# Performance work log

Measured on AMD Instinct MI355X. Metric: run time of the kernel, lower is better.

Reference implementation:

```python
import jax, jax.numpy as jnp
import numpy as np

B, S, C_IN, C_OUT = 8, 2048, 512, 512

def setup_inputs() -> dict:
    key = jax.random.key(0)
    k1, k2, k3, k4 = jax.random.split(key, 4)
    sc = 1.0 / np.sqrt(C_IN)
    return {
        "x": jax.random.normal(k1, (B, S, C_IN), dtype=jnp.float32),
        "Wq": jax.random.normal(k2, (C_OUT, C_IN), dtype=jnp.float32) * sc,
        "Wk": jax.random.normal(k3, (C_OUT, C_IN), dtype=jnp.float32) * sc,
        "Wv": jax.random.normal(k4, (C_OUT, C_IN), dtype=jnp.float32) * sc,
    }

def reference(x, Wq, Wk, Wv):
    # x: [B,S,Cin]; weights [Cout,Cin] (torch Linear convention, no bias)
    C = Wq.shape[0]
    dk = jnp.sqrt(jnp.float32(1.0) / C)  # torch: sqrt(1/out_features)
    q = jnp.einsum('bsi,oi->bso', x, Wq)
    k = jnp.einsum('bsi,oi->bso', x, Wk)
    v = jnp.einsum('bsi,oi->bso', x, Wv)
    phi_q = jax.nn.elu(q * dk) + 1.0
    phi_k = jax.nn.elu(k * dk) + 1.0
    b = x.shape[0]
    mem0 = jnp.zeros((b, C, C), x.dtype)   # running sum of phi_k v^T
    zeta0 = jnp.zeros((b, C), x.dtype)     # running sum of phi_k
    def step(carry, inp):
        mem, zeta = carry
        pq, pk, vv = inp                    # each [B,C]
        dm = pk[:, :, None] * vv[:, None, :]              # [B,C,C]
        scale = jnp.einsum('bc,bc->b', pq, pk + zeta) + 1e-5
        num = jnp.einsum('bc,bcd->bd', pq, dm + mem)
        y = num / scale[:, None]
        # state updates are under torch.no_grad -> detach
        new_mem = jax.lax.stop_gradient(mem + dm)
        new_zeta = jax.lax.stop_gradient(zeta + pk)
        return (new_mem, new_zeta), y
    xs = (phi_q.transpose(1, 0, 2), phi_k.transpose(1, 0, 2), v.transpose(1, 0, 2))
    _, ys = jax.lax.scan(step, (mem0, zeta0), xs)  # ys: [S,B,C]
    return ys.transpose(1, 0, 2)                   # [B,S,C]
```

## Files before the change

### kernel.cpp

```cpp
#include <hip/hip_runtime.h>


constexpr int Bn  = 8;
constexpr int Sn  = 2048;
constexpr int Cn  = 512;
constexpr int Tn  = 128;
constexpr int NCn = 16;
constexpr float DKf = 0.04419417382415922f;

typedef __attribute__((ext_vector_type(8))) short bf16x8;
typedef __attribute__((ext_vector_type(4))) float f32x4;

__device__ __forceinline__ unsigned short f2bf(float f) {
  unsigned u = __float_as_uint(f);
  u = (u + 0x7fffu + ((u >> 16) & 1u)) >> 16;
  return (unsigned short)u;
}
__device__ __forceinline__ float bf2f(unsigned short h) {
  return __uint_as_float(((unsigned)h) << 16);
}
__device__ __forceinline__ float phi_f(float u) {
  float s = u * DKf;
  return s > 0.0f ? s + 1.0f : __expf(s);
}

__device__ __forceinline__ void stage128x32(const unsigned short* __restrict__ g,
                                            int ld, unsigned short* lds,
                                            int wid, int lane) {
#pragma unroll
  for (int cc = 0; cc < 2; ++cc) {
    const int row = cc * 64 + wid * 16 + (lane >> 2);
    const int ks  = (lane & 3) ^ ((row >> 1) & 3);
    const unsigned short* src = g + (size_t)row * ld + ks * 8;
    unsigned short* dst = lds + (size_t)(cc * 256 + wid * 64) * 8;
    __builtin_amdgcn_global_load_lds(
        (const __attribute__((address_space(1))) void*)src,
        (__attribute__((address_space(3))) void*)dst, 16, 0, 0);
  }
}

__device__ __forceinline__ void mm_loop(const unsigned short* __restrict__ Ag, int lda,
                                        const unsigned short* __restrict__ Bg, int ldb,
                                        int nkt,
                                        unsigned short* Al, unsigned short* Bl,
                                        f32x4 acc[4][4]) {
  const int t = threadIdx.x, wid = t >> 6, lane = t & 63;
  const int wm = wid >> 1, wn = wid & 1;
  const int fr = lane & 15, kb = lane >> 4;
  for (int kt = 0; kt < nkt; ++kt) {
    __syncthreads();
    stage128x32(Ag + kt * 32, lda, Al, wid, lane);
    stage128x32(Bg + kt * 32, ldb, Bl, wid, lane);
    __syncthreads();
    bf16x8 af[4], bf[4];
#pragma unroll
    for (int m = 0; m < 4; ++m) {
      const int r = wm * 64 + m * 16 + fr;
      af[m] = *(const bf16x8*)&Al[r * 32 + ((kb ^ ((r >> 1) & 3)) << 3)];
    }
#pragma unroll
    for (int n = 0; n < 4; ++n) {
      const int r = wn * 64 + n * 16 + fr;
      bf[n] = *(const bf16x8*)&Bl[r * 32 + ((kb ^ ((r >> 1) & 3)) << 3)];
    }
#pragma unroll
    for (int m = 0; m < 4; ++m)
#pragma unroll
      for (int n = 0; n < 4; ++n)
        acc[m][n] = __builtin_amdgcn_mfma_f32_16x16x32_bf16(af[m], bf[n], acc[m][n], 0, 0, 0);
  }
}

__global__ __launch_bounds__(256) void k_cast_x(const float* __restrict__ x,
                                                unsigned short* __restrict__ xb) {
  const size_t i8 = ((size_t)blockIdx.x * 256 + threadIdx.x) * 8;
  float4 a = *(const float4*)&x[i8];
  float4 b = *(const float4*)&x[i8 + 4];
  uint4 o;
  o.x = (unsigned)f2bf(a.x) | ((unsigned)f2bf(a.y) << 16);
  o.y = (unsigned)f2bf(a.z) | ((unsigned)f2bf(a.w) << 16);
  o.z = (unsigned)f2bf(b.x) | ((unsigned)f2bf(b.y) << 16);
  o.w = (unsigned)f2bf(b.z) | ((unsigned)f2bf(b.w) << 16);
  *(uint4*)&xb[i8] = o;
}

__global__ __launch_bounds__(256) void k_cast_w(const float* __restrict__ Wq,
                                                const float* __restrict__ Wk,
                                                const float* __restrict__ Wv,
                                                unsigned short* __restrict__ Wb) {
  const int z = blockIdx.y;
  const float* __restrict__ src = (z == 0) ? Wq : (z == 1 ? Wk : Wv);
  const size_t i8 = ((size_t)blockIdx.x * 256 + threadIdx.x) * 8;
  float4 a = *(const float4*)&src[i8];
  float4 b = *(const float4*)&src[i8 + 4];
  uint4 o;
  o.x = (unsigned)f2bf(a.x) | ((unsigned)f2bf(a.y) << 16);
  o.y = (unsigned)f2bf(a.z) | ((unsigned)f2bf(a.w) << 16);
  o.z = (unsigned)f2bf(b.x) | ((unsigned)f2bf(b.y) << 16);
  o.w = (unsigned)f2bf(b.z) | ((unsigned)f2bf(b.w) << 16);
  *(uint4*)&Wb[(size_t)z * Cn * Cn + i8] = o;
}

__global__ __launch_bounds__(256) void k_proj(
    const unsigned short* __restrict__ xb, const unsigned short* __restrict__ Wb,
    unsigned short* __restrict__ PQ, unsigned short* __restrict__ PK,
    unsigned short* __restrict__ PKt, unsigned short* __restrict__ Vt,
    float* __restrict__ zsum)
{
  __shared__ unsigned short Al[128 * 32], Bl[128 * 32];
  __shared__ float zbuf[2][128];
  const int bid = blockIdx.x;
  const int xcd = bid & 7, idx = bid >> 3;
  const int n = idx & 3, z = (idx >> 2) % 3, mloc = idx / 12;
  const int n0 = n * 128, m0 = (xcd * 16 + mloc) * 128;
  const int t = threadIdx.x, wid = t >> 6, lane = t & 63;
  const int wm = wid >> 1, wn = wid & 1;
  f32x4 acc[4][4];
  const f32x4 zero = {0.f, 0.f, 0.f, 0.f};
#pragma unroll
  for (int m = 0; m < 4; ++m)
#pragma unroll
    for (int nn = 0; nn < 4; ++nn) acc[m][nn] = zero;

  mm_loop(xb + (size_t)m0 * Cn, Cn,
          Wb + (size_t)z * Cn * Cn + (size_t)n0 * Cn, Cn, Cn / 32, Al, Bl, acc);

  float ps[4] = {0.f, 0.f, 0.f, 0.f};
#pragma unroll
  for (int m = 0; m < 4; ++m)
#pragma unroll
    for (int nn = 0; nn < 4; ++nn) {
      const int row0 = m0 + wm * 64 + m * 16 + ((lane >> 4) << 2);
      const int col  = n0 + wn * 64 + nn * 16 + (lane & 15);
      f32x4 v = acc[m][nn];
      if (z == 0) {
#pragma unroll
        for (int j = 0; j < 4; ++j)
          PQ[(size_t)(row0 + j) * Cn + col] = f2bf(phi_f(v[j]));
      } else if (z == 1) {
        ushort4 p;
#pragma unroll
        for (int j = 0; j < 4; ++j) {
          unsigned short u = f2bf(phi_f(v[j]));
          PK[(size_t)(row0 + j) * Cn + col] = u;
          (&p.x)[j] = u;
          ps[nn] += bf2f(u);
        }
        const int b = row0 >> 11, tq = row0 & (Sn - 1);
        *(ushort4*)&PKt[((size_t)b * Cn + col) * Sn + tq] = p;
      } else {
        ushort4 p;
#pragma unroll
        for (int j = 0; j < 4; ++j) (&p.x)[j] = f2bf(v[j]);
        const int b = row0 >> 11, tq = row0 & (Sn - 1);
        *(ushort4*)&Vt[((size_t)b * Cn + col) * Sn + tq] = p;
      }
    }

  if (z == 1) {
#pragma unroll
    for (int nn = 0; nn < 4; ++nn) {
      float v = ps[nn];
      v += __shfl_xor(v, 16); v += __shfl_xor(v, 32);
      if (lane < 16) zbuf[wm][wn * 64 + nn * 16 + lane] = v;
    }
    __syncthreads();
    if (t < 128) {
      const int b = m0 >> 11, ch = (m0 >> 7) & 15;
      zsum[((size_t)b * NCn + ch) * Cn + n0 + t] = zbuf[0][t] + zbuf[1][t];
    }
  }
}

__global__ __launch_bounds__(256) void k_gram(
    const unsigned short* __restrict__ PQ, const unsigned short* __restrict__ PK,
    unsigned short* __restrict__ Abuf, float* __restrict__ scale)
{
  __shared__ unsigned short Al[128 * 32], Bl[128 * 32];
  __shared__ float rsmem[2][128];
  const int b = blockIdx.y, ch = blockIdx.x;
  const size_t base = ((size_t)b * Sn + ch * Tn) * Cn;
  f32x4 acc[4][4];
  const f32x4 zero = {0.f, 0.f, 0.f, 0.f};
#pragma unroll
  for (int m = 0; m < 4; ++m)
#pragma unroll
    for (int n = 0; n < 4; ++n) acc[m][n] = zero;

  mm_loop(PQ + base, Cn, PK + base, Cn, Cn / 32, Al, Bl, acc);

  const int t = threadIdx.x, wid = t >> 6, lane = t & 63;
  const int wm = wid >> 1, wn = wid & 1;
  float rsum[4][4];
#pragma unroll
  for (int m = 0; m < 4; ++m)
#pragma unroll
    for (int j = 0; j < 4; ++j) rsum[m][j] = 0.f;
#pragma unroll
  for (int m = 0; m < 4; ++m)
#pragma unroll
    for (int n = 0; n < 4; ++n) {
      f32x4 v = acc[m][n];
#pragma unroll
      for (int j = 0; j < 4; ++j) {
        const int row = wm * 64 + m * 16 + ((lane >> 4) << 2) + j;
        const int col = wn * 64 + n * 16 + (lane & 15);
        unsigned short u = (col <= row) ? f2bf(v[j]) : 0;
        Abuf[((size_t)(b * NCn + ch) * Tn + row) * Tn + col] = u;
        rsum[m][j] += bf2f(u);
      }
    }
#pragma unroll
  for (int m = 0; m < 4; ++m)
#pragma unroll
    for (int j = 0; j < 4; ++j) {
      float r = rsum[m][j];
      r += __shfl_xor(r, 1); r += __shfl_xor(r, 2);
      r += __shfl_xor(r, 4); r += __shfl_xor(r, 8);
      if ((lane & 15) == 0)
        rsmem[wn][wm * 64 + m * 16 + ((lane >> 4) << 2) + j] = r;
    }
  __syncthreads();
  if (t < 128)
    scale[(size_t)b * Sn + ch * Tn + t] = rsmem[0][t] + rsmem[1][t];
}

__global__ __launch_bounds__(512) void k_zpre(const float* __restrict__ zsum,
                                              float* __restrict__ zpre) {
  const int b = blockIdx.x, c = threadIdx.x;
  float run = 0.f;
  for (int ch = 0; ch < NCn; ++ch) {
    zpre[((size_t)b * NCn + ch) * Cn + c] = run;
    run += zsum[((size_t)b * NCn + ch) * Cn + c];
  }
}

__global__ __launch_bounds__(256) void k_scale(const unsigned short* __restrict__ PQ,
                                               const float* __restrict__ zpre,
                                               float* __restrict__ scale) {
  const int b = blockIdx.y;
  const int w = threadIdx.x >> 6, lane = threadIdx.x & 63;
  const int row = blockIdx.x * 4 + w;
  const int ch = row >> 7;
  const unsigned short* pq = PQ + ((size_t)b * Sn + row) * Cn + lane * 8;
  const float* zp = zpre + ((size_t)b * NCn + ch) * Cn + lane * 8;
  uint4 q = *(const uint4*)pq;
  float4 z0 = *(const float4*)zp, z1 = *(const float4*)(zp + 4);
  float d = bf2f((unsigned short)(q.x & 0xffff)) * z0.x
          + bf2f((unsigned short)(q.x >> 16))    * z0.y
          + bf2f((unsigned short)(q.y & 0xffff)) * z0.z
          + bf2f((unsigned short)(q.y >> 16))    * z0.w
          + bf2f((unsigned short)(q.z & 0xffff)) * z1.x
          + bf2f((unsigned short)(q.z >> 16))    * z1.y
          + bf2f((unsigned short)(q.w & 0xffff)) * z1.z
          + bf2f((unsigned short)(q.w >> 16))    * z1.w;
#pragma unroll
  for (int off = 32; off > 0; off >>= 1) d += __shfl_xor(d, off);
  if (lane == 0) scale[(size_t)b * Sn + row] += d + 1e-5f;
}

__device__ __forceinline__ void stage64x128(const unsigned short* __restrict__ g,
                                            int ld, unsigned short* lds,
                                            int wid, int lane) {
#pragma unroll
  for (int i = 0; i < 4; ++i) {
    const int row = wid * 16 + i * 4 + (lane >> 4);
    const int s   = (lane & 15) ^ (row & 7);
    const unsigned short* src = g + (size_t)row * ld + s * 8;
    unsigned short* dst = lds + (size_t)(wid * 16 + i * 4) * 128;
    __builtin_amdgcn_global_load_lds(
        (const __attribute__((address_space(1))) void*)src,
        (__attribute__((address_space(3))) void*)dst, 16, 0, 0);
  }
}

__global__ __launch_bounds__(256) void k_kvp(
    const unsigned short* __restrict__ PKt, const unsigned short* __restrict__ Vt,
    unsigned short* __restrict__ Mpre)
{
  __shared__ unsigned short Al[64 * 128], Bl[64 * 128];
  const int bid = blockIdx.x;
  const int b = bid & 7, idx = bid >> 3;
  const int d0 = (idx & 7) * 64, c0 = (idx >> 3) * 64;
  const int t = threadIdx.x, wid = t >> 6, lane = t & 63;
  const int wm = wid >> 1, wn = wid & 1;
  const int fr = lane & 15, kb = lane >> 4;
  f32x4 acc[2][2];
  const f32x4 zero = {0.f, 0.f, 0.f, 0.f};
#pragma unroll
  for (int m = 0; m < 2; ++m)
#pragma unroll
    for (int n = 0; n < 2; ++n) acc[m][n] = zero;
  const unsigned short* Ag = PKt + ((size_t)b * Cn + c0) * Sn;
  const unsigned short* Bg = Vt  + ((size_t)b * Cn + d0) * Sn;
  for (int ch = 0; ch < NCn; ++ch) {
    if (ch > 0) {
#pragma unroll
      for (int m = 0; m < 2; ++m)
#pragma unroll
        for (int n = 0; n < 2; ++n) {
          const int c_row = c0 + wm * 32 + m * 16 + (kb << 2);
          const int d     = d0 + wn * 32 + n * 16 + fr;
          ushort4 p;
#pragma unroll
          for (int j = 0; j < 4; ++j) (&p.x)[j] = f2bf(acc[m][n][j]);
          *(ushort4*)&Mpre[((size_t)(b * NCn + ch) * Cn + d) * Cn + c_row] = p;
        }
    }
    __syncthreads();
    stage64x128(Ag + ch * Tn, Sn, Al, wid, lane);
    stage64x128(Bg + ch * Tn, Sn, Bl, wid, lane);
    __syncthreads();
#pragma unroll
    for (int kt = 0; kt < 4; ++kt) {
      bf16x8 af[2], bf[2];
#pragma unroll
      for (int m = 0; m < 2; ++m) {
        const int r = wm * 32 + m * 16 + fr;
        af[m] = *(const bf16x8*)&Al[r * 128 + (((kt * 4 + kb) ^ (r & 7)) << 3)];
      }
#pragma unroll
      for (int n = 0; n < 2; ++n) {
        const int r = wn * 32 + n * 16 + fr;
        bf[n] = *(const bf16x8*)&Bl[r * 128 + (((kt * 4 + kb) ^ (r & 7)) << 3)];
      }
#pragma unroll
      for (int m = 0; m < 2; ++m)
#pragma unroll
        for (int n = 0; n < 2; ++n)
          acc[m][n] = __builtin_amdgcn_mfma_f32_16x16x32_bf16(af[m], bf[n], acc[m][n], 0, 0, 0);
    }
  }
}

__global__ __launch_bounds__(256) void k_avinter(
    const unsigned short* __restrict__ Abuf, const unsigned short* __restrict__ Vt,
    const unsigned short* __restrict__ PQ, const unsigned short* __restrict__ Mpre,
    const float* __restrict__ scale, float* __restrict__ out)
{
  __shared__ unsigned short Al[128 * 32], Bl[128 * 32];
  const int bid = blockIdx.x;
  const int logical = (bid & 7) * 64 + (bid >> 3);
  const int d0 = (logical & 3) * 128;
  const int ch = (logical >> 2) & 15;
  const int b  = logical >> 6;
  const int t0 = ch * Tn;
  f32x4 acc[4][4];
  const f32x4 zero = {0.f, 0.f, 0.f, 0.f};
#pragma unroll
  for (int m = 0; m < 4; ++m)
#pragma unroll
    for (int n = 0; n < 4; ++n) acc[m][n] = zero;

  mm_loop(Abuf + (size_t)(b * NCn + ch) * Tn * Tn, Tn,
          Vt + ((size_t)b * Cn + d0) * Sn + t0, Sn, Tn / 32, Al, Bl, acc);
  if (ch > 0)
    mm_loop(PQ + ((size_t)b * Sn + t0) * Cn, Cn,
            Mpre + ((size_t)(b * NCn + ch) * Cn + d0) * Cn, Cn, Cn / 32, Al, Bl, acc);

  const int t = threadIdx.x, wid = t >> 6, lane = t & 63;
  const int wm = wid >> 1, wn = wid & 1;
#pragma unroll
  for (int m = 0; m < 4; ++m)
#pragma unroll
    for (int n = 0; n < 4; ++n) {
      const int row0 = t0 + wm * 64 + m * 16 + ((lane >> 4) << 2);
      const int col  = d0 + wn * 64 + n * 16 + (lane & 15);
      f32x4 v = acc[m][n];
#pragma unroll
      for (int j = 0; j < 4; ++j) {
        const size_t sidx = (size_t)b * Sn + row0 + j;
        out[sidx * Cn + col] = v[j] / scale[sidx];
      }
    }
}

extern "C" void kernel_launch(void* const* d_in, const int* in_sizes, int n_in,
                              void* d_out, int out_size, void* d_ws, size_t ws_size,
                              hipStream_t stream)
{
  const float* x  = (const float*)d_in[0];
  const float* Wq = (const float*)d_in[1];
  const float* Wk = (const float*)d_in[2];
  const float* Wv = (const float*)d_in[3];
  float* out = (float*)d_out;

  unsigned short* xb   = (unsigned short*)d_ws;
  unsigned short* Wb   = xb   + (size_t)Bn * Sn * Cn;
  unsigned short* PQ   = Wb   + (size_t)3 * Cn * Cn;
  unsigned short* PK   = PQ   + (size_t)Bn * Sn * Cn;
  unsigned short* PKt  = PK   + (size_t)Bn * Sn * Cn;
  unsigned short* Vt   = PKt  + (size_t)Bn * Sn * Cn;
  unsigned short* Abuf = Vt   + (size_t)Bn * Sn * Cn;
  unsigned short* Mpre = Abuf + (size_t)Bn * NCn * Tn * Tn;
  float* scale = (float*)(Mpre + (size_t)Bn * NCn * Cn * Cn);
  float* zsum  = scale + (size_t)Bn * Sn;
  float* zpre  = zsum  + (size_t)Bn * NCn * Cn;
  (void)ws_size; (void)in_sizes; (void)n_in; (void)out_size;

  hipLaunchKernelGGL(k_cast_x, dim3(4096), dim3(256), 0, stream, x, xb);
  hipLaunchKernelGGL(k_cast_w, dim3(128, 3), dim3(256), 0, stream, Wq, Wk, Wv, Wb);
  hipLaunchKernelGGL(k_proj, dim3(1536), dim3(256), 0, stream, xb, Wb, PQ, PK, PKt, Vt, zsum);
  hipLaunchKernelGGL(k_zpre, dim3(Bn), dim3(512), 0, stream, zsum, zpre);
  hipLaunchKernelGGL(k_gram, dim3(NCn, Bn), dim3(256), 0, stream, PQ, PK, Abuf, scale);
  hipLaunchKernelGGL(k_scale, dim3(Sn / 4, Bn), dim3(256), 0, stream, PQ, zpre, scale);
  hipLaunchKernelGGL(k_kvp, dim3(512), dim3(256), 0, stream, PKt, Vt, Mpre);
  hipLaunchKernelGGL(k_avinter, dim3(512), dim3(256), 0, stream, Abuf, Vt, PQ, Mpre, scale, out);
}
```

Measured before the change: 139.8 us.

## Double-buffer LDS tiles in GEMM loops to overlap global loads with MFMA

Both the shared mm_loop helper and the k_kvp kernel now use two LDS buffers per operand. The next K-tile (or chunk) is staged with global_load_lds while MFMAs run on the current buffer, and there is one barrier per iteration instead of two. The aim is to hide global-to-LDS latency behind matrix compute in the projection, gram, chunk-state and output kernels. It doubles LDS usage per block, which could reduce occupancy. It also relies on the barrier's wait to complete the asynchronous prefetch before the buffer is read.

New measurement: 138.6 us. No clear change (-0.9%).

```diff
diff --git a/kernel.cpp b/kernel.cpp
--- a/kernel.cpp
+++ b/kernel.cpp
@@ -47,27 +47,36 @@
   const int t = threadIdx.x, wid = t >> 6, lane = t & 63;
   const int wm = wid >> 1, wn = wid & 1;
   const int fr = lane & 15, kb = lane >> 4;
+  stage128x32(Ag, lda, Al, wid, lane);
+  stage128x32(Bg, ldb, Bl, wid, lane);
+  __syncthreads();
+  int cur = 0;
   for (int kt = 0; kt < nkt; ++kt) {
-    __syncthreads();
-    stage128x32(Ag + kt * 32, lda, Al, wid, lane);
-    stage128x32(Bg + kt * 32, ldb, Bl, wid, lane);
-    __syncthreads();
+    const int nxt = cur ^ 1;
+    if (kt + 1 < nkt) {
+      stage128x32(Ag + (kt + 1) * 32, lda, Al + nxt * 4096, wid, lane);
+      stage128x32(Bg + (kt + 1) * 32, ldb, Bl + nxt * 4096, wid, lane);
+    }
+    const unsigned short* Ac = Al + cur * 4096;
+    const unsigned short* Bc = Bl + cur * 4096;
     bf16x8 af[4], bf[4];
 #pragma unroll
     for (int m = 0; m < 4; ++m) {
       const int r = wm * 64 + m * 16 + fr;
-      af[m] = *(const bf16x8*)&Al[r * 32 + ((kb ^ ((r >> 1) & 3)) << 3)];
+      af[m] = *(const bf16x8*)&Ac[r * 32 + ((kb ^ ((r >> 1) & 3)) << 3)];
     }
 #pragma unroll
     for (int n = 0; n < 4; ++n) {
       const int r = wn * 64 + n * 16 + fr;
-      bf[n] = *(const bf16x8*)&Bl[r * 32 + ((kb ^ ((r >> 1) & 3)) << 3)];
+      bf[n] = *(const bf16x8*)&Bc[r * 32 + ((kb ^ ((r >> 1) & 3)) << 3)];
     }
 #pragma unroll
     for (int m = 0; m < 4; ++m)
 #pragma unroll
       for (int n = 0; n < 4; ++n)
         acc[m][n] = __builtin_amdgcn_mfma_f32_16x16x32_bf16(af[m], bf[n], acc[m][n], 0, 0, 0);
+    __syncthreads();
+    cur = nxt;
   }
 }
 
@@ -107,7 +116,7 @@
     unsigned short* __restrict__ PKt, unsigned short* __restrict__ Vt,
     float* __restrict__ zsum)
 {
-  __shared__ unsigned short Al[128 * 32], Bl[128 * 32];
+  __shared__ unsigned short Al[2 * 128 * 32], Bl[2 * 128 * 32];
   __shared__ float zbuf[2][128];
   const int bid = blockIdx.x;
   const int xcd = bid & 7, idx = bid >> 3;
@@ -176,7 +185,7 @@
     const unsigned short* __restrict__ PQ, const unsigned short* __restrict__ PK,
     unsigned short* __restrict__ Abuf, float* __restrict__ scale)
 {
-  __shared__ unsigned short Al[128 * 32], Bl[128 * 32];
+  __shared__ unsigned short Al[2 * 128 * 32], Bl[2 * 128 * 32];
   __shared__ float rsmem[2][128];
   const int b = blockIdx.y, ch = blockIdx.x;
   const size_t base = ((size_t)b * Sn + ch * Tn) * Cn;
@@ -278,7 +287,7 @@
     const unsigned short* __restrict__ PKt, const unsigned short* __restrict__ Vt,
     unsigned short* __restrict__ Mpre)
 {
-  __shared__ unsigned short Al[64 * 128], Bl[64 * 128];
+  __shared__ unsigned short Al[2 * 64 * 128], Bl[2 * 64 * 128];
   const int bid = blockIdx.x;
   const int b = bid & 7, idx = bid >> 3;
   const int d0 = (idx & 7) * 64, c0 = (idx >> 3) * 64;
@@ -293,7 +302,16 @@
     for (int n = 0; n < 2; ++n) acc[m][n] = zero;
   const unsigned short* Ag = PKt + ((size_t)b * Cn + c0) * Sn;
   const unsigned short* Bg = Vt  + ((size_t)b * Cn + d0) * Sn;
+  stage64x128(Ag, Sn, Al, wid, lane);
+  stage64x128(Bg, Sn, Bl, wid, lane);
+  __syncthreads();
+  int cur = 0;
   for (int ch = 0; ch < NCn; ++ch) {
+    const int nxt = cur ^ 1;
+    if (ch + 1 < NCn) {
+      stage64x128(Ag + (ch + 1) * Tn, Sn, Al + nxt * 8192, wid, lane);
+      stage64x128(Bg + (ch + 1) * Tn, Sn, Bl + nxt * 8192, wid, lane);
+    }
     if (ch > 0) {
 #pragma unroll
       for (int m = 0; m < 2; ++m)
@@ -307,22 +325,20 @@
           *(ushort4*)&Mpre[((size_t)(b * NCn + ch) * Cn + d) * Cn + c_row] = p;
         }
     }
-    __syncthreads();
-    stage64x128(Ag + ch * Tn, Sn, Al, wid, lane);
-    stage64x128(Bg + ch * Tn, Sn, Bl, wid, lane);
-    __syncthreads();
+    const unsigned short* Ac = Al + cur * 8192;
+    const unsigned short* Bc = Bl + cur * 8192;
 #pragma unroll
     for (int kt = 0; kt < 4; ++kt) {
       bf16x8 af[2], bf[2];
 #pragma unroll
       for (int m = 0; m < 2; ++m) {
         const int r = wm * 32 + m * 16 + fr;
-        af[m] = *(const bf16x8*)&Al[r * 128 + (((kt * 4 + kb) ^ (r & 7)) << 3)];
+        af[m] = *(const bf16x8*)&Ac[r * 128 + (((kt * 4 + kb) ^ (r & 7)) << 3)];
       }
 #pragma unroll
       for (int n = 0; n < 2; ++n) {
         const int r = wn * 32 + n * 16 + fr;
-        bf[n] = *(const bf16x8*)&Bl[r * 128 + (((kt * 4 + kb) ^ (r & 7)) << 3)];
+        bf[n] = *(const bf16x8*)&Bc[r * 128 + (((kt * 4 + kb) ^ (r & 7)) << 3)];
       }
 #pragma unroll
       for (int m = 0; m < 2; ++m)
@@ -330,6 +346,8 @@
         for (int n = 0; n < 2; ++n)
           acc[m][n] = __builtin_amdgcn_mfma_f32_16x16x32_bf16(af[m], bf[n], acc[m][n], 0, 0, 0);
     }
+    __syncthreads();
+    cur = nxt;
   }
 }
 
@@ -338,7 +356,7 @@
     const unsigned short* __restrict__ PQ, const unsigned short* __restrict__ Mpre,
     const float* __restrict__ scale, float* __restrict__ out)
 {
-  __shared__ unsigned short Al[128 * 32], Bl[128 * 32];
+  __shared__ unsigned short Al[2 * 128 * 32], Bl[2 * 128 * 32];
   const int bid = blockIdx.x;
   const int logical = (bid & 7) * 64 + (bid >> 3);
   const int d0 = (logical & 3) * 128;
```
